# Optimization experiments

Hardware: AMD Instinct MI355X
Metric: run time of the kernel (lower is better)

Reference implementation:

```python
import jax, jax.numpy as jnp
import numpy as np

HEADS = 8
DIM_HEAD = 64
EPS = 1e-05


def _layernorm(t, scale):
    # flax LayerNorm with use_bias=False: (t - mean) / sqrt(var + eps) * scale
    mu = jnp.mean(t, axis=-1, keepdims=True)
    var = jnp.var(t, axis=-1, keepdims=True)
    return (t - mu) * jax.lax.rsqrt(var + EPS) * scale


def setup_inputs() -> dict:
    key = jax.random.key(0)
    ks = jax.random.split(key, 5)
    B, H, W, C = 32, 32, 32, 512
    dim = HEADS * DIM_HEAD  # 512
    x = jax.random.normal(ks[0], (B, H, W, C), dtype=jnp.float32)
    ln1_scale = jnp.ones((C,), dtype=jnp.float32)
    # 1x1 convs == channel matmuls; kernels stored as [in, out]
    w_qkv = jax.random.normal(ks[1], (C, dim * 3), dtype=jnp.float32) * 0.02
    w_out = jax.random.normal(ks[2], (dim, C), dtype=jnp.float32) * 0.02
    b_out = jnp.zeros((C,), dtype=jnp.float32)
    ln2_scale = jnp.ones((C,), dtype=jnp.float32)
    return {"x": x, "ln1_scale": ln1_scale, "w_qkv": w_qkv,
            "w_out": w_out, "b_out": b_out, "ln2_scale": ln2_scale}


def reference(x, ln1_scale, w_qkv, w_out, b_out, ln2_scale):
    B, H, W, C = x.shape
    N = H * W
    dim = HEADS * DIM_HEAD

    normed = _layernorm(x, ln1_scale)                       # [B,H,W,C]
    qkv = jnp.einsum('bxyc,cf->bxyf', normed, w_qkv)        # 1x1 conv, no bias
    q, k, v = jnp.split(qkv, 3, axis=-1)
    q = q.reshape(B, N, HEADS, DIM_HEAD)
    k = k.reshape(B, N, HEADS, DIM_HEAD)
    v = v.reshape(B, N, HEADS, DIM_HEAD)

    q = jax.nn.softmax(q, axis=-1) / jnp.sqrt(jnp.asarray(DIM_HEAD, x.dtype))
    k = jax.nn.softmax(k, axis=1)   # softmax over the token axis (axis=-3)
    v = v / N

    # linear attention: context = k^T v, then out = q . context
    context = jnp.einsum('bnhd,bnhe->bhde', k, v)           # [B,h,d,e]
    out = jnp.einsum('bhde,bnhd->bnhe', context, q)         # == 'b h e n' transposed
    out = out.reshape(B, H, W, dim)

    out = jnp.einsum('bxyf,fc->bxyc', out, w_out) + b_out   # 1x1 conv with bias
    out = _layernorm(out, ln2_scale)                        # to_out.norm_0
    return out + x
```

## Files before the change

### kernel.cpp

```cpp
#include <hip/hip_runtime.h>
#include <stdint.h>

typedef _Float16 h8 __attribute__((ext_vector_type(8)));
typedef _Float16 h4v __attribute__((ext_vector_type(4)));
typedef float f32x4 __attribute__((ext_vector_type(4)));

__device__ __forceinline__ float clampf(float x, float lo, float hi) {
    return fminf(fmaxf(x, lo), hi);
}
__device__ __forceinline__ void gload16(const _Float16* g, _Float16* l) {
    __builtin_amdgcn_global_load_lds(
        (const __attribute__((address_space(1))) unsigned int*)g,
        (__attribute__((address_space(3))) unsigned int*)l, 16, 0, 0);
}

__global__ __launch_bounds__(256) void transpose_f2h(const float* __restrict__ in,
                                                     _Float16* __restrict__ out,
                                                     int rows, int cols) {
    __shared__ _Float16 tile[32][33];
    int bx = blockIdx.x * 32, by = blockIdx.y * 32;
    int tx = threadIdx.x & 31, ty = threadIdx.x >> 5;
    for (int i = ty; i < 32; i += 8)
        tile[i][tx] = (_Float16)in[(size_t)(by + i) * cols + bx + tx];
    __syncthreads();
    for (int i = ty; i < 32; i += 8)
        out[(size_t)(bx + i) * rows + by + tx] = tile[tx][i];
}

__global__ __launch_bounds__(256) void ln1_kernel(const float* __restrict__ x,
                                                  const float* __restrict__ scale,
                                                  _Float16* __restrict__ out) {
    int row = blockIdx.x * 4 + (threadIdx.x >> 6);
    int lane = threadIdx.x & 63;
    const float4* xp = (const float4*)(x + (size_t)row * 512 + lane * 8);
    float4 a = xp[0], b = xp[1];
    const float4* sp = (const float4*)(scale + lane * 8);
    float4 s0v = sp[0], s1v = sp[1];
    float f[8] = {a.x, a.y, a.z, a.w, b.x, b.y, b.z, b.w};
    float sc[8] = {s0v.x, s0v.y, s0v.z, s0v.w, s1v.x, s1v.y, s1v.z, s1v.w};
    float s = 0.f, ss = 0.f;
#pragma unroll
    for (int j = 0; j < 8; j++) { s += f[j]; ss += f[j] * f[j]; }
#pragma unroll
    for (int off = 1; off < 64; off <<= 1) { s += __shfl_xor(s, off); ss += __shfl_xor(ss, off); }
    float mean = s * (1.f / 512.f);
    float var  = ss * (1.f / 512.f) - mean * mean;
    float rs   = rsqrtf(fmaxf(var, 0.f) + 1e-5f);
    union { uint4 u; _Float16 h[8]; } ov;
#pragma unroll
    for (int j = 0; j < 8; j++) ov.h[j] = (_Float16)((f[j] - mean) * rs * sc[j]);
    *(uint4*)(out + (size_t)row * 512 + lane * 8) = ov.u;
}

__global__ __launch_bounds__(512) void gemm_kvexp(const _Float16* __restrict__ A,
                                                  const _Float16* __restrict__ BT,
                                                  _Float16* __restrict__ ekT,
                                                  _Float16* __restrict__ vT,
                                                  float* __restrict__ Sbuf) {
    __shared__ __attribute__((aligned(16))) char smem[40960];
    _Float16* As = (_Float16*)smem;
    _Float16* Bs = (_Float16*)(smem + 8192);
    _Float16* tr = (_Float16*)smem;
    int t = threadIdx.x, w = t >> 6, lane = t & 63;
    int lm = lane & 15, q4 = lane >> 4;
    int m0 = blockIdx.y * 128, n0 = blockIdx.x * 512;
    int wm = (w & 1) * 64, wn = (w >> 1) * 128;
    f32x4 acc[4][8];
#pragma unroll
    for (int i = 0; i < 4; i++)
#pragma unroll
        for (int j = 0; j < 8; j++) acc[i][j] = (f32x4){0.f, 0.f, 0.f, 0.f};

    int sr = t >> 2, sc = (t & 3) * 8;
    const _Float16* Ag = A + (size_t)(m0 + sr) * 512 + sc;
    const _Float16* Bg = BT + (size_t)(n0 + sr) * 512 + sc;
    _Float16* AsW = As + w * 512;

    for (int k0 = 0; k0 < 512; k0 += 32) {
        gload16(Ag + k0, AsW);
#pragma unroll
        for (int j = 0; j < 4; j++)
            gload16(Bg + (size_t)j * 128 * 512 + k0, Bs + j * 4096 + w * 512);
        __syncthreads();
        h8 af[4], bf[8];
#pragma unroll
        for (int i = 0; i < 4; i++) af[i] = *(const h8*)(As + (wm + i * 16 + lm) * 32 + q4 * 8);
#pragma unroll
        for (int i = 0; i < 8; i++) bf[i] = *(const h8*)(Bs + (wn + i * 16 + lm) * 32 + q4 * 8);
#pragma unroll
        for (int mi = 0; mi < 4; mi++)
#pragma unroll
            for (int ni = 0; ni < 8; ni++)
                acc[mi][ni] = __builtin_amdgcn_mfma_f32_16x16x32_f16(bf[ni], af[mi], acc[mi][ni], 0, 0, 0);
        __syncthreads();
    }
    bool isK = (n0 < 512);
    int bl = m0 >> 10, nl0 = m0 & 1023;
    int nw = w >> 1;
    int oc = t >> 2, qtr = t & 3;
#pragma unroll
    for (int g = 0; g < 4; g++) {
        __syncthreads();
        if (nw == g) {
#pragma unroll
            for (int mi = 0; mi < 4; mi++) {
                int row = wm + mi * 16 + lm;
#pragma unroll
                for (int ni = 0; ni < 8; ni++) {
                    int lc = ni * 16 + q4 * 4;
                    f32x4 v = acc[mi][ni];
#pragma unroll
                    for (int r = 0; r < 4; r++) {
                        float f = v[r];
                        if (isK) f = __expf(clampf(f, -30.f, 30.f));
                        tr[(lc + r) * 132 + row] = (_Float16)f;
                    }
                }
            }
        }
        __syncthreads();
        int c = n0 + g * 128 + oc;
        int h = (c >> 6) & 7, de = c & 63;
        _Float16* dst = (isK ? ekT : vT)
                        + ((size_t)(bl * 8 + h) * 64 + de) * 1024 + nl0 + qtr * 32;
        const _Float16* src = tr + oc * 132 + qtr * 32;
        float ssum = 0.f;
#pragma unroll
        for (int j = 0; j < 4; j++) {
            h4v u0 = *(const h4v*)(src + j * 8);
            h4v u1 = *(const h4v*)(src + j * 8 + 4);
            if (isK) {
#pragma unroll
                for (int q = 0; q < 4; q++) ssum += (float)u0[q] + (float)u1[q];
            }
            union { struct { h4v a, b; } hh; uint4 u; } uu;
            uu.hh.a = u0; uu.hh.b = u1;
            *(uint4*)(dst + j * 8) = uu.u;
        }
        if (isK) {
            ssum += __shfl_xor(ssum, 1);
            ssum += __shfl_xor(ssum, 2);
            if (qtr == 0) atomicAdd(&Sbuf[(bl * 8 + h) * 64 + de], ssum);
        }
    }
}

__global__ __launch_bounds__(512) void ctx_gemm(const _Float16* __restrict__ ekT,
                                                const _Float16* __restrict__ vT,
                                                float* __restrict__ part) {
    __shared__ __attribute__((aligned(16))) _Float16 As[64 * 32];
    __shared__ __attribute__((aligned(16))) _Float16 Bs[64 * 32];
    int t = threadIdx.x, w = t >> 6, lane = t & 63;
    int lm = lane & 15, q4 = lane >> 4;
    int bhl = blockIdx.x;
    int wd = (w & 3) * 16, we = (w >> 2) * 32;
    int tl = t & 255;
    int sr = tl >> 2, sc = (tl & 3) * 8;
    const _Float16* G = (t >= 256 ? vT : ekT) + (size_t)bhl * 65536 + (size_t)sr * 1024 + sc;
    _Float16* LW = (t >= 256 ? Bs : As) + (w & 3) * 512;
    f32x4 acc[2];
    acc[0] = (f32x4){0.f, 0.f, 0.f, 0.f};
    acc[1] = (f32x4){0.f, 0.f, 0.f, 0.f};

    for (int k0 = 0; k0 < 1024; k0 += 32) {
        gload16(G + k0, LW);
        __syncthreads();
        h8 af = *(const h8*)(As + (wd + lm) * 32 + q4 * 8);
#pragma unroll
        for (int nt = 0; nt < 2; nt++) {
            h8 bf = *(const h8*)(Bs + (we + nt * 16 + lm) * 32 + q4 * 8);
            acc[nt] = __builtin_amdgcn_mfma_f32_16x16x32_f16(bf, af, acc[nt], 0, 0, 0);
        }
        __syncthreads();
    }
    float* dst = part + (size_t)bhl * 4096 + (wd + lm) * 64 + we;
#pragma unroll
    for (int nt = 0; nt < 2; nt++)
        *(f32x4*)(dst + nt * 16 + q4 * 4) = acc[nt];
}

__global__ __launch_bounds__(256) void gemm_qattn(const _Float16* __restrict__ A,
                                                  const _Float16* __restrict__ BT,
                                                  const float* __restrict__ part,
                                                  const float* __restrict__ Sbuf,
                                                  _Float16* __restrict__ attn) {
    __shared__ __attribute__((aligned(16))) char smem[33792 + 17408];
    _Float16* As  = (_Float16*)smem;
    _Float16* Bs  = (_Float16*)(smem + 8192);
    _Float16* qn  = (_Float16*)smem;
    _Float16* csT = (_Float16*)(smem + 33792);
    int t = threadIdx.x, w = t >> 6, lane = t & 63;
    int lm = lane & 15, q4 = lane >> 4;
    int m0 = blockIdx.y * 128, n0 = blockIdx.x * 128;
    int wm = (w & 1) * 64, wn = (w >> 1) * 64;
    f32x4 acc[4][4];
#pragma unroll
    for (int i = 0; i < 4; i++)
#pragma unroll
        for (int j = 0; j < 4; j++) acc[i][j] = (f32x4){0.f, 0.f, 0.f, 0.f};

    int sr = t >> 2, sc = (t & 3) * 8;
    const _Float16* Ag = A + (size_t)(m0 + sr) * 512 + sc;
    const _Float16* Bg = BT + (size_t)(n0 + sr) * 512 + sc;
    _Float16* AsW = As + w * 512;
    _Float16* BsW = Bs + w * 512;

    for (int k0 = 0; k0 < 512; k0 += 32) {
        gload16(Ag + k0, AsW);
        gload16(Ag + (size_t)64 * 512 + k0, AsW + 64 * 32);
        gload16(Bg + k0, BsW);
        gload16(Bg + (size_t)64 * 512 + k0, BsW + 64 * 32);
        __syncthreads();
        h8 af[4], bf[4];
#pragma unroll
        for (int i = 0; i < 4; i++) af[i] = *(const h8*)(As + (wm + i * 16 + lm) * 32 + q4 * 8);
#pragma unroll
        for (int i = 0; i < 4; i++) bf[i] = *(const h8*)(Bs + (wn + i * 16 + lm) * 32 + q4 * 8);
#pragma unroll
        for (int mi = 0; mi < 4; mi++)
#pragma unroll
            for (int ni = 0; ni < 4; ni++)
                acc[mi][ni] = __builtin_amdgcn_mfma_f32_16x16x32_f16(bf[ni], af[mi], acc[mi][ni], 0, 0, 0);
        __syncthreads();
    }
    float rws[4];
#pragma unroll
    for (int mi = 0; mi < 4; mi++) {
        float s = 0.f;
#pragma unroll
        for (int ni = 0; ni < 4; ni++) {
            f32x4 e;
#pragma unroll
            for (int r = 0; r < 4; r++) {
                e[r] = __expf(clampf(acc[mi][ni][r], -30.f, 30.f));
                s += e[r];
            }
            acc[mi][ni] = e;
        }
        s += __shfl_xor(s, 16);
        s += __shfl_xor(s, 32);
        rws[mi] = 1.f / (s * 8.f);
    }
#pragma unroll
    for (int mi = 0; mi < 4; mi++) {
        int row = wm + mi * 16 + lm;
        float r = rws[mi];
#pragma unroll
        for (int ni = 0; ni < 4; ni++) {
            int col0 = wn + ni * 16 + q4 * 4;
            h4v o;
#pragma unroll
            for (int j = 0; j < 4; j++) o[j] = (_Float16)(acc[mi][ni][j] * r);
            *(h4v*)(qn + row * 132 + col0) = o;
        }
    }
    int bl = m0 >> 10;
    int head0 = n0 >> 6;
#pragma unroll
    for (int hh2 = 0; hh2 < 2; hh2++) {
        int bh = bl * 8 + head0 + hh2;
        const f32x4* p0 = (const f32x4*)(part + (size_t)bh * 4096);
        for (int i = t; i < 1024; i += 256) {
            f32x4 v = p0[i];
            int d = i >> 4, e0 = (i & 15) * 4;
            float is = 1.f / Sbuf[bh * 64 + d];
#pragma unroll
            for (int j = 0; j < 4; j++)
                csT[hh2 * 64 * 68 + (e0 + j) * 68 + d] = (_Float16)(v[j] * is);
        }
    }
    __syncthreads();
    int hh = w >> 1;
    f32x4 acc2[4][4];
#pragma unroll
    for (int i = 0; i < 4; i++)
#pragma unroll
        for (int j = 0; j < 4; j++) acc2[i][j] = (f32x4){0.f, 0.f, 0.f, 0.f};
#pragma unroll
    for (int kc = 0; kc < 2; kc++) {
        h8 af[4], bf[4];
#pragma unroll
        for (int mi = 0; mi < 4; mi++) {
            const _Float16* p = qn + (wm + mi * 16 + lm) * 132 + hh * 64 + kc * 32 + q4 * 8;
            h4v lo = *(const h4v*)p;
            h4v hi = *(const h4v*)(p + 4);
            h8 a;
#pragma unroll
            for (int j = 0; j < 4; j++) { a[j] = lo[j]; a[4 + j] = hi[j]; }
            af[mi] = a;
        }
#pragma unroll
        for (int ni = 0; ni < 4; ni++) {
            const _Float16* p = csT + hh * 64 * 68 + (ni * 16 + lm) * 68 + kc * 32 + q4 * 8;
            h4v lo = *(const h4v*)p;
            h4v hi = *(const h4v*)(p + 4);
            h8 b;
#pragma unroll
            for (int j = 0; j < 4; j++) { b[j] = lo[j]; b[4 + j] = hi[j]; }
            bf[ni] = b;
        }
#pragma unroll
        for (int mi = 0; mi < 4; mi++)
#pragma unroll
            for (int ni = 0; ni < 4; ni++)
                acc2[mi][ni] = __builtin_amdgcn_mfma_f32_16x16x32_f16(bf[ni], af[mi], acc2[mi][ni], 0, 0, 0);
    }
#pragma unroll
    for (int mi = 0; mi < 4; mi++) {
        int row = m0 + wm + mi * 16 + lm;
#pragma unroll
        for (int ni = 0; ni < 4; ni++) {
            int col0 = n0 + wn + ni * 16 + q4 * 4;
            h4v o;
#pragma unroll
            for (int r = 0; r < 4; r++) o[r] = (_Float16)acc2[mi][ni][r];
            *(h4v*)(attn + (size_t)row * 512 + col0) = o;
        }
    }
}

__global__ __launch_bounds__(512) void gemm_projln2(const _Float16* __restrict__ A,
                                                    const _Float16* __restrict__ BT,
                                                    const float* __restrict__ bias,
                                                    const float* __restrict__ x,
                                                    const float* __restrict__ scale,
                                                    float* __restrict__ out) {
    __shared__ __attribute__((aligned(16))) _Float16 As[128 * 32];
    __shared__ __attribute__((aligned(16))) _Float16 Bs[512 * 32];
    __shared__ float rs_sum[2][64][4];
    __shared__ float rs_ssq[2][64][4];
    int t = threadIdx.x, w = t >> 6, lane = t & 63;
    int lm = lane & 15, q4 = lane >> 4;
    int m0 = blockIdx.x * 128;
    int wm = (w & 1) * 64, wn = (w >> 1) * 128;
    f32x4 acc[4][8];
#pragma unroll
    for (int i = 0; i < 4; i++)
#pragma unroll
        for (int j = 0; j < 8; j++) acc[i][j] = (f32x4){0.f, 0.f, 0.f, 0.f};

    int sr = t >> 2, sc = (t & 3) * 8;
    const _Float16* Ag = A + (size_t)(m0 + sr) * 512 + sc;
    const _Float16* Bg = BT + (size_t)sr * 512 + sc;
    _Float16* AsW = As + w * 512;

    for (int k0 = 0; k0 < 512; k0 += 32) {
        gload16(Ag + k0, AsW);
#pragma unroll
        for (int j = 0; j < 4; j++)
            gload16(Bg + (size_t)j * 128 * 512 + k0, Bs + j * 4096 + w * 512);
        __syncthreads();
        h8 af[4], bf[8];
#pragma unroll
        for (int i = 0; i < 4; i++) af[i] = *(const h8*)(As + (wm + i * 16 + lm) * 32 + q4 * 8);
#pragma unroll
        for (int i = 0; i < 8; i++) bf[i] = *(const h8*)(Bs + (wn + i * 16 + lm) * 32 + q4 * 8);
#pragma unroll
        for (int mi = 0; mi < 4; mi++)
#pragma unroll
            for (int ni = 0; ni < 8; ni++)
                acc[mi][ni] = __builtin_amdgcn_mfma_f32_16x16x32_f16(bf[ni], af[mi], acc[mi][ni], 0, 0, 0);
        __syncthreads();
    }
    const float os = 1.f / 1024.f;
    int mwi = w & 1, nwi = w >> 1;
#pragma unroll
    for (int mi = 0; mi < 4; mi++) {
        float s = 0.f, ss = 0.f;
#pragma unroll
        for (int ni = 0; ni < 8; ni++) {
            float4 b4 = *(const float4*)(bias + wn + ni * 16 + q4 * 4);
            const float* bp = &b4.x;
#pragma unroll
            for (int r = 0; r < 4; r++) {
                float v = acc[mi][ni][r] * os + bp[r];
                acc[mi][ni][r] = v;
                s += v; ss += v * v;
            }
        }
        s  += __shfl_xor(s, 16);  s  += __shfl_xor(s, 32);
        ss += __shfl_xor(ss, 16); ss += __shfl_xor(ss, 32);
        if (q4 == 0) {
            rs_sum[mwi][mi * 16 + lm][nwi] = s;
            rs_ssq[mwi][mi * 16 + lm][nwi] = ss;
        }
    }
    __syncthreads();
#pragma unroll
    for (int mi = 0; mi < 4; mi++) {
        int r64 = mi * 16 + lm;
        float s  = rs_sum[mwi][r64][0] + rs_sum[mwi][r64][1] + rs_sum[mwi][r64][2] + rs_sum[mwi][r64][3];
        float ss = rs_ssq[mwi][r64][0] + rs_ssq[mwi][r64][1] + rs_ssq[mwi][r64][2] + rs_ssq[mwi][r64][3];
        float mean = s * (1.f / 512.f);
        float var  = ss * (1.f / 512.f) - mean * mean;
        float rstd = rsqrtf(fmaxf(var, 0.f) + 1e-5f);
        int row = m0 + wm + r64;
#pragma unroll
        for (int ni = 0; ni < 8; ni++) {
            int col0 = wn + ni * 16 + q4 * 4;
            float4 sc4 = *(const float4*)(scale + col0);
            float4 x4  = *(const float4*)(x + (size_t)row * 512 + col0);
            const float* scp = &sc4.x; const float* xp = &x4.x;
            float4 o;
            float* op = &o.x;
#pragma unroll
            for (int r = 0; r < 4; r++)
                op[r] = (acc[mi][ni][r] - mean) * rstd * scp[r] + xp[r];
            *(float4*)(out + (size_t)row * 512 + col0) = o;
        }
    }
}

extern "C" void kernel_launch(void* const* d_in, const int* in_sizes, int n_in,
                              void* d_out, int out_size, void* d_ws, size_t ws_size,
                              hipStream_t stream) {
    const float* x    = (const float*)d_in[0];
    const float* ln1s = (const float*)d_in[1];
    const float* wqkv = (const float*)d_in[2];
    const float* wout = (const float*)d_in[3];
    const float* bout = (const float*)d_in[4];
    const float* ln2s = (const float*)d_in[5];
    float* out = (float*)d_out;

    char* ws = (char*)d_ws;
    _Float16* wqkvT  = (_Float16*)(ws);
    _Float16* woutT  = (_Float16*)(ws + 1572864);
    float*    part   = (float*)(ws + 2097152);
    float*    Sbuf   = (float*)(ws + 6291456);
    _Float16* normed = (_Float16*)(ws + 6356992);
    _Float16* attnF  = (_Float16*)(ws + 39911424);
    _Float16* ekT = (_Float16*)d_out;
    _Float16* vT  = (_Float16*)((char*)d_out + 33554432);

    transpose_f2h<<<dim3(48, 16), 256, 0, stream>>>(wqkv, wqkvT, 512, 1536);
    transpose_f2h<<<dim3(16, 16), 256, 0, stream>>>(wout, woutT, 512, 512);
    ln1_kernel<<<8192, 256, 0, stream>>>(x, ln1s, normed);
    hipMemsetAsync(Sbuf, 0, 65536, stream);

    gemm_kvexp<<<dim3(2, 256), 512, 0, stream>>>(normed, wqkvT + 512 * 512, ekT, vT, Sbuf);
    ctx_gemm<<<256, 512, 0, stream>>>(ekT, vT, part);
    gemm_qattn<<<dim3(4, 256), 256, 0, stream>>>(normed, wqkvT, part, Sbuf, attnF);
    gemm_projln2<<<256, 512, 0, stream>>>(attnF, woutT, bout, x, ln2s, out);
}
```

Measured before the change: 303.4 us.

## Swap GEMM operand roles in kv kernel to store transposed outputs directly

The kv GEMM now tiles 128 output channels by 512 tokens, with weights as the small operand and normalized activations as the large one. Each accumulator fragment then maps onto a contiguous run of tokens in the channel-major ekT/vT layout, so results are written straight from registers. This drops the shared-memory transpose stage and its extra barriers. The trade-off is narrower 8-byte stores instead of 16-byte ones, plus a different grid shape and reuse pattern: weight tiles are now reread by 64 token blocks.

```diff
diff --git a/kernel.cpp b/kernel.cpp
--- a/kernel.cpp
+++ b/kernel.cpp
@@ -57,14 +57,12 @@
                                                   _Float16* __restrict__ ekT,
                                                   _Float16* __restrict__ vT,
                                                   float* __restrict__ Sbuf) {
-    __shared__ __attribute__((aligned(16))) char smem[40960];
-    _Float16* As = (_Float16*)smem;
-    _Float16* Bs = (_Float16*)(smem + 8192);
-    _Float16* tr = (_Float16*)smem;
+    __shared__ __attribute__((aligned(16))) _Float16 Ws[128 * 32];
+    __shared__ __attribute__((aligned(16))) _Float16 Ns[512 * 32];
     int t = threadIdx.x, w = t >> 6, lane = t & 63;
     int lm = lane & 15, q4 = lane >> 4;
-    int m0 = blockIdx.y * 128, n0 = blockIdx.x * 512;
-    int wm = (w & 1) * 64, wn = (w >> 1) * 128;
+    int n0 = blockIdx.x * 512, c0 = blockIdx.y * 128;
+    int wc = (w & 1) * 64, wn = (w >> 1) * 128;
     f32x4 acc[4][8];
 #pragma unroll
     for (int i = 0; i < 4; i++)
@@ -72,75 +70,56 @@
         for (int j = 0; j < 8; j++) acc[i][j] = (f32x4){0.f, 0.f, 0.f, 0.f};
 
     int sr = t >> 2, sc = (t & 3) * 8;
-    const _Float16* Ag = A + (size_t)(m0 + sr) * 512 + sc;
-    const _Float16* Bg = BT + (size_t)(n0 + sr) * 512 + sc;
-    _Float16* AsW = As + w * 512;
+    const _Float16* Wg = BT + (size_t)(c0 + sr) * 512 + sc;
+    const _Float16* Ng = A + (size_t)(n0 + sr) * 512 + sc;
+    _Float16* WsW = Ws + w * 512;
 
     for (int k0 = 0; k0 < 512; k0 += 32) {
-        gload16(Ag + k0, AsW);
+        gload16(Wg + k0, WsW);
 #pragma unroll
         for (int j = 0; j < 4; j++)
-            gload16(Bg + (size_t)j * 128 * 512 + k0, Bs + j * 4096 + w * 512);
-        __syncthreads();
-        h8 af[4], bf[8];
-#pragma unroll
-        for (int i = 0; i < 4; i++) af[i] = *(const h8*)(As + (wm + i * 16 + lm) * 32 + q4 * 8);
-#pragma unroll
-        for (int i = 0; i < 8; i++) bf[i] = *(const h8*)(Bs + (wn + i * 16 + lm) * 32 + q4 * 8);
-#pragma unroll
-        for (int mi = 0; mi < 4; mi++)
-#pragma unroll
-            for (int ni = 0; ni < 8; ni++)
-                acc[mi][ni] = __builtin_amdgcn_mfma_f32_16x16x32_f16(bf[ni], af[mi], acc[mi][ni], 0, 0, 0);
-        __syncthreads();
-    }
-    bool isK = (n0 < 512);
-    int bl = m0 >> 10, nl0 = m0 & 1023;
-    int nw = w >> 1;
-    int oc = t >> 2, qtr = t & 3;
-#pragma unroll
-    for (int g = 0; g < 4; g++) {
-        __syncthreads();
-        if (nw == g) {
-#pragma unroll
-            for (int mi = 0; mi < 4; mi++) {
-                int row = wm + mi * 16 + lm;
-#pragma unroll
-                for (int ni = 0; ni < 8; ni++) {
-                    int lc = ni * 16 + q4 * 4;
-                    f32x4 v = acc[mi][ni];
-#pragma unroll
-                    for (int r = 0; r < 4; r++) {
-                        float f = v[r];
-                        if (isK) f = __expf(clampf(f, -30.f, 30.f));
-                        tr[(lc + r) * 132 + row] = (_Float16)f;
-                    }
-                }
+            gload16(Ng + (size_t)j * 128 * 512 + k0, Ns + j * 4096 + w * 512);
+        __syncthreads();
+        h8 wf[4], nf[8];
+#pragma unroll
+        for (int i = 0; i < 4; i++) wf[i] = *(const h8*)(Ws + (wc + i * 16 + lm) * 32 + q4 * 8);
+#pragma unroll
+        for (int i = 0; i < 8; i++) nf[i] = *(const h8*)(Ns + (wn + i * 16 + lm) * 32 + q4 * 8);
+#pragma unroll
+        for (int ci = 0; ci < 4; ci++)
+#pragma unroll
+            for (int nj = 0; nj < 8; nj++)
+                acc[ci][nj] = __builtin_amdgcn_mfma_f32_16x16x32_f16(nf[nj], wf[ci], acc[ci][nj], 0, 0, 0);
+        __syncthreads();
+    }
+    bool isK = (c0 < 512);
+    int bl = n0 >> 10;
+    int nl0 = (n0 & 1023) + wn;
+    _Float16* obase = isK ? ekT : vT;
+#pragma unroll
+    for (int ci = 0; ci < 4; ci++) {
+        int c_abs = c0 + wc + ci * 16 + lm;
+        int h = (c_abs >> 6) & 7, de = c_abs & 63;
+        _Float16* rowp = obase + ((size_t)(bl * 8 + h) * 64 + de) * 1024 + nl0;
+        float ssum = 0.f;
+#pragma unroll
+        for (int nj = 0; nj < 8; nj++) {
+            f32x4 v = acc[ci][nj];
+            h4v o;
+#pragma unroll
+            for (int r = 0; r < 4; r++) {
+                float f = v[r];
+                if (isK) f = __expf(clampf(f, -30.f, 30.f));
+                _Float16 e = (_Float16)f;
+                o[r] = e;
+                ssum += (float)e;
             }
-        }
-        __syncthreads();
-        int c = n0 + g * 128 + oc;
-        int h = (c >> 6) & 7, de = c & 63;
-        _Float16* dst = (isK ? ekT : vT)
-                        + ((size_t)(bl * 8 + h) * 64 + de) * 1024 + nl0 + qtr * 32;
-        const _Float16* src = tr + oc * 132 + qtr * 32;
-        float ssum = 0.f;
-#pragma unroll
-        for (int j = 0; j < 4; j++) {
-            h4v u0 = *(const h4v*)(src + j * 8);
-            h4v u1 = *(const h4v*)(src + j * 8 + 4);
-            if (isK) {
-#pragma unroll
-                for (int q = 0; q < 4; q++) ssum += (float)u0[q] + (float)u1[q];
-            }
-            union { struct { h4v a, b; } hh; uint4 u; } uu;
-            uu.hh.a = u0; uu.hh.b = u1;
-            *(uint4*)(dst + j * 8) = uu.u;
+            *(h4v*)(rowp + nj * 16 + q4 * 4) = o;
         }
         if (isK) {
-            ssum += __shfl_xor(ssum, 1);
-            ssum += __shfl_xor(ssum, 2);
-            if (qtr == 0) atomicAdd(&Sbuf[(bl * 8 + h) * 64 + de], ssum);
+            ssum += __shfl_xor(ssum, 16);
+            ssum += __shfl_xor(ssum, 32);
+            if (q4 == 0) atomicAdd(&Sbuf[(bl * 8 + h) * 64 + de], ssum);
         }
     }
 }
@@ -437,7 +416,7 @@
     ln1_kernel<<<8192, 256, 0, stream>>>(x, ln1s, normed);
     hipMemsetAsync(Sbuf, 0, 65536, stream);
 
-    gemm_kvexp<<<dim3(2, 256), 512, 0, stream>>>(normed, wqkvT + 512 * 512, ekT, vT, Sbuf);
+    gemm_kvexp<<<dim3(64, 8), 512, 0, stream>>>(normed, wqkvT + 512 * 512, ekT, vT, Sbuf);
     ctx_gemm<<<256, 512, 0, stream>>>(ekT, vT, part);
     gemm_qattn<<<dim3(4, 256), 256, 0, stream>>>(normed, wqkvT, part, Sbuf, attnF);
     gemm_projln2<<<256, 512, 0, stream>>>(attnF, woutT, bout, x, ln2s, out);
```

Result: faster. 290.7 us (-4.2%).
